# Kernel tuning notes

Measured on AMD Instinct MI355X. Metric: run time of the kernel, lower is better.

The kernel has to match this reference:

```python
import jax, jax.numpy as jnp
import numpy as np

B, T, C, H, HS = 2, 2048, 1024, 16, 64


def setup_inputs() -> dict:
    key = jax.random.key(0)
    ks = jax.random.split(key, 7)
    x = jax.random.normal(ks[0], (B, T, C), dtype=jnp.float32)
    # causal mask, broadcast over batch (True = attend)
    attention_mask = jnp.broadcast_to(jnp.tril(jnp.ones((T, T), dtype=bool)), (B, T, T))
    s = 1.0 / np.sqrt(C)
    wq = jax.random.normal(ks[1], (H, C, HS), dtype=jnp.float32) * s   # per-head query Linear (no bias)
    wk = jax.random.normal(ks[2], (H, C, HS), dtype=jnp.float32) * s
    wv = jax.random.normal(ks[3], (H, C, HS), dtype=jnp.float32) * s
    wproj = jax.random.normal(ks[4], (H * HS, C), dtype=jnp.float32) * (1.0 / np.sqrt(H * HS))
    bproj = jnp.zeros((C,), dtype=jnp.float32)
    return {"x": x, "attention_mask": attention_mask,
            "wq": wq, "wk": wk, "wv": wv, "wproj": wproj, "bproj": bproj}


def reference(x, attention_mask, wq, wk, wv, wproj, bproj):
    # per-head projections: [B,H,T,HS]
    q = jnp.einsum('btc,hcd->bhtd', x, wq)
    k = jnp.einsum('btc,hcd->bhtd', x, wk)
    v = jnp.einsum('btc,hcd->bhtd', x, wv)
    scale = 1.0 / jnp.sqrt(jnp.asarray(HS, dtype=x.dtype))
    wei = jnp.einsum('bhtd,bhsd->bhts', q, k) * scale          # [B,H,T,T]
    wei = jnp.where(attention_mask[:, None, :, :], wei, -jnp.inf)
    wei = jax.nn.softmax(wei, axis=-1)
    out = jnp.einsum('bhts,bhsd->bhtd', wei, v)                 # [B,H,T,HS]
    out = out.transpose(0, 2, 1, 3).reshape(B, T, H * HS)       # concat heads
    return out @ wproj + bproj                                  # [B,T,C]
```

## Files before the change

### kernel.cpp

```cpp
#include <hip/hip_runtime.h>
#include <math.h>

typedef float f32x4 __attribute__((ext_vector_type(4)));
typedef __bf16 bf16x8 __attribute__((ext_vector_type(8)));
typedef unsigned short u16x8 __attribute__((ext_vector_type(8)));
typedef unsigned short u16x4 __attribute__((ext_vector_type(4)));

#define DEV static __device__ __forceinline__

DEV unsigned short f2bf(float f) {
    unsigned int u = __builtin_bit_cast(unsigned int, f);
    u += 0x7fffu + ((u >> 16) & 1u);
    return (unsigned short)(u >> 16);
}

#define GLD16(gp, lp) __builtin_amdgcn_global_load_lds( \
    (__attribute__((address_space(1))) void*)(gp),      \
    (__attribute__((address_space(3))) void*)(lp), 16, 0, 0)

#define WAITBAR(N) asm volatile("s_waitcnt vmcnt(" #N ")\n\ts_barrier" ::: "memory")
#define BARRIER()  asm volatile("s_barrier" ::: "memory")

__global__ __launch_bounds__(256) void k_prep(const float* __restrict__ x,
                                              const float* __restrict__ wq,
                                              const float* __restrict__ wk,
                                              const float* __restrict__ wv,
                                              const float* __restrict__ wproj,
                                              unsigned short* __restrict__ xb,
                                              unsigned short* __restrict__ WqkvT,
                                              unsigned short* __restrict__ WprojT) {
    const int bid = blockIdx.x, tid = threadIdx.x;
    if (bid < 2048) {
        int i = bid * 256 + tid;
        const float4* p = (const float4*)(x + (size_t)i * 8);
        float4 a = p[0], b = p[1];
        u16x8 o;
        o[0] = f2bf(a.x); o[1] = f2bf(a.y); o[2] = f2bf(a.z); o[3] = f2bf(a.w);
        o[4] = f2bf(b.x); o[5] = f2bf(b.y); o[6] = f2bf(b.z); o[7] = f2bf(b.w);
        *(u16x8*)(xb + (size_t)i * 8) = o;
        return;
    }
    __shared__ unsigned short t[64][68];
    if (bid < 2816) {
        int zb = bid - 2048;
        int z = zb >> 4, wsel = z >> 4, zz = z & 15;
        const float* src = (wsel == 0 ? wq : wsel == 1 ? wk : wv) + (size_t)zz * 65536;
        int r0 = (zb & 15) * 64;
#pragma unroll
        for (int it = 0; it < 4; ++it) {
            int r = (tid >> 4) + it * 16;
            int c4 = (tid & 15) * 4;
            float4 v = *(const float4*)&src[(size_t)(r0 + r) * 64 + c4];
            t[c4 + 0][r] = f2bf(v.x);
            t[c4 + 1][r] = f2bf(v.y);
            t[c4 + 2][r] = f2bf(v.z);
            t[c4 + 3][r] = f2bf(v.w);
        }
        __syncthreads();
#pragma unroll
        for (int it = 0; it < 4; ++it) {
            int c = (tid >> 4) + it * 16;
            int r4 = (tid & 15) * 4;
            u16x4 o;
            o[0] = t[c][r4 + 0]; o[1] = t[c][r4 + 1];
            o[2] = t[c][r4 + 2]; o[3] = t[c][r4 + 3];
            int row = wsel * 1024 + zz * 64 + c;
            *(u16x4*)&WqkvT[(size_t)row * 1024 + r0 + r4] = o;
        }
    } else {
        int zb = bid - 2816;
        int r0 = (zb & 15) * 64, c0 = (zb >> 4) * 64;
#pragma unroll
        for (int it = 0; it < 4; ++it) {
            int r = (tid >> 4) + it * 16;
            int c4 = (tid & 15) * 4;
            float4 v = *(const float4*)&wproj[(size_t)(r0 + r) * 1024 + c0 + c4];
            t[c4 + 0][r] = f2bf(v.x);
            t[c4 + 1][r] = f2bf(v.y);
            t[c4 + 2][r] = f2bf(v.z);
            t[c4 + 3][r] = f2bf(v.w);
        }
        __syncthreads();
#pragma unroll
        for (int it = 0; it < 4; ++it) {
            int c = (tid >> 4) + it * 16;
            int r4 = (tid & 15) * 4;
            u16x4 o;
            o[0] = t[c][r4 + 0]; o[1] = t[c][r4 + 1];
            o[2] = t[c][r4 + 2]; o[3] = t[c][r4 + 3];
            *(u16x4*)&WprojT[(size_t)(c0 + c) * 1024 + r0 + r4] = o;
        }
    }
}

template <int STAGE, int M_REP, int NB, int SUPM, int SUPN>
__global__ __launch_bounds__(256) void k_gemm(const unsigned short* __restrict__ A,
                                              const unsigned short* __restrict__ Bt,
                                              int Kd,
                                              float* __restrict__ outF,
                                              const float* __restrict__ bias,
                                              unsigned short* __restrict__ Qb,
                                              unsigned short* __restrict__ Kb,
                                              unsigned short* __restrict__ Vt) {
    constexpr int BM = M_REP * 32;
    __shared__ unsigned short As[2][BM * 64] __attribute__((aligned(16)));
    __shared__ unsigned short Bs[2][128 * 64] __attribute__((aligned(16)));
    const int tid = threadIdx.x, l = tid & 63, w = tid >> 6;
    constexpr int BN_CH = NB / SUPN;
    const int orig = blockIdx.x;
    const int xcd = orig & 7, sdx = orig >> 3;
    const int bm = (xcd / BN_CH) * SUPM + (sdx % SUPM);
    const int bn = (xcd % BN_CH) * SUPN + (sdx / SUPM);
    const int wr = w >> 1, wc = w & 1;
    const int g = l >> 4, q = l & 15;
    f32x4 acc[M_REP][4] = {};
    const unsigned short* gA = A + (size_t)(bm * BM + w * 8 + (l >> 3)) * Kd + (l & 7) * 8;
    const unsigned short* gB = Bt + (size_t)(bn * 128 + w * 8 + (l >> 3)) * Kd + (l & 7) * 8;

#define GSTAGE(buf, k0) do {                                                  \
        _Pragma("unroll")                                                     \
        for (int it = 0; it < M_REP; ++it)                                    \
            GLD16(gA + (size_t)(it * 32) * Kd + (k0), &As[buf][(it * 32 + w * 8) * 64]); \
        _Pragma("unroll")                                                     \
        for (int it = 0; it < 4; ++it)                                        \
            GLD16(gB + (size_t)(it * 32) * Kd + (k0), &Bs[buf][(it * 32 + w * 8) * 64]); \
    } while (0)

    const int nt = Kd >> 6;
    GSTAGE(0, 0);
    int cur = 0;
    for (int t = 0; t < nt; ++t) {
        if (t + 1 < nt) {
            GSTAGE(cur ^ 1, (t + 1) << 6);
            if constexpr (M_REP == 4) WAITBAR(8); else WAITBAR(6);
        } else {
            WAITBAR(0);
        }
#pragma unroll
        for (int ks = 0; ks < 2; ++ks) {
            bf16x8 af[M_REP], bfr[4];
#pragma unroll
            for (int mi = 0; mi < M_REP; ++mi)
                af[mi] = *(const bf16x8*)&As[cur][(wr * (M_REP * 16) + mi * 16 + q) * 64 + ks * 32 + g * 8];
#pragma unroll
            for (int ni = 0; ni < 4; ++ni)
                bfr[ni] = *(const bf16x8*)&Bs[cur][(wc * 64 + ni * 16 + q) * 64 + ks * 32 + g * 8];
#pragma unroll
            for (int mi = 0; mi < M_REP; ++mi)
#pragma unroll
                for (int ni = 0; ni < 4; ++ni)
                    acc[mi][ni] = __builtin_amdgcn_mfma_f32_16x16x32_bf16(
                        af[mi], bfr[ni], acc[mi][ni], 0, 0, 0);
        }
        BARRIER();
        cur ^= 1;
    }
#undef GSTAGE
#pragma unroll
    for (int mi = 0; mi < M_REP; ++mi)
#pragma unroll
        for (int ni = 0; ni < 4; ++ni)
#pragma unroll
            for (int r = 0; r < 4; ++r) {
                float c = acc[mi][ni][r];
                int m = bm * BM + wr * (M_REP * 16) + mi * 16 + g * 4 + r;
                int n = bn * 128 + wc * 64 + ni * 16 + q;
                if (STAGE == 1) {
                    int b = m >> 11, t = m & 2047;
                    int proj = n >> 10, rr = n & 1023, h = rr >> 6, d = rr & 63;
                    int bh = b * 16 + h;
                    if (proj == 0)
                        Qb[((size_t)bh * 2048 + t) * 64 + d] = f2bf(c * 0.18033688011112042f);
                    else if (proj == 1)
                        Kb[((size_t)bh * 2048 + t) * 64 + d] = f2bf(c);
                    else
                        Vt[((size_t)bh * 64 + d) * 2048 + t] = f2bf(c);
                } else {
                    outF[(size_t)m * 1024 + n] = c + bias[n];
                }
            }
}

__global__ __launch_bounds__(256) void k_attn(const unsigned short* __restrict__ Qb,
                                              const unsigned short* __restrict__ Kb,
                                              const unsigned short* __restrict__ Vt,
                                              unsigned short* __restrict__ att) {
    __shared__ unsigned short Ks[2][2][4096] __attribute__((aligned(16)));
    __shared__ unsigned short Vs[2][2][4096] __attribute__((aligned(16)));
    __shared__ unsigned short P[4][16][72];
    const int tid = threadIdx.x, l = tid & 63, w = tid >> 6;
    const int pj = blockIdx.x, bh = blockIdx.y;
    const int b = bh >> 4, h = bh & 15;
    const int ql = l & 15, g = l >> 4;
    const unsigned short* Qp = Qb + (size_t)bh * 2048 * 64;
    const unsigned short* Kp = Kb + (size_t)bh * 2048 * 64;
    const unsigned short* Vp = Vt + (size_t)bh * 64 * 2048;

    const int sr0 = w * 16 + (l >> 3);
    const int sch = (l & 7) ^ (l >> 3);
    const unsigned short* gK0 = Kp + (size_t)sr0 * 64 + sch * 8;
    const unsigned short* gK1 = gK0 + 8 * 64;
    const unsigned short* gV0 = Vp + (size_t)sr0 * 2048 + sch * 8;
    const unsigned short* gV1 = gV0 + 8 * 2048;

#define ATT_STAGE(buf, kvb) do {                                                  \
        GLD16(gK0 + (size_t)(kvb) * 64, &Ks[buf][0][(w * 16) * 64]);              \
        GLD16(gK1 + (size_t)(kvb) * 64, &Ks[buf][0][(w * 16 + 8) * 64]);          \
        GLD16(gK0 + (size_t)((kvb) + 64) * 64, &Ks[buf][1][(w * 16) * 64]);       \
        GLD16(gK1 + (size_t)((kvb) + 64) * 64, &Ks[buf][1][(w * 16 + 8) * 64]);   \
        GLD16(gV0 + (kvb), &Vs[buf][0][(w * 16) * 64]);                           \
        GLD16(gV1 + (kvb), &Vs[buf][0][(w * 16 + 8) * 64]);                       \
        GLD16(gV0 + (kvb) + 64, &Vs[buf][1][(w * 16) * 64]);                      \
        GLD16(gV1 + (kvb) + 64, &Vs[buf][1][(w * 16 + 8) * 64]);                  \
    } while (0)

    for (int ph = 0; ph < 2; ++ph) {
        const int qt = ph ? (31 - pj) : pj;
        const int qg = qt * 64 + w * 16 + ql;
        const int minqg = qt * 64 + w * 16;
        const int nkv2 = (qt + 2) >> 1;

        bf16x8 qf0 = *(const bf16x8*)(Qp + (size_t)qg * 64 + g * 8);
        bf16x8 qf1 = *(const bf16x8*)(Qp + (size_t)qg * 64 + 32 + g * 8);
        f32x4 ot[4] = {};
        float mrun = -1e30f, lsum = 0.f;

        ATT_STAGE(0, 0);
        int cur = 0;

        for (int kb = 0; kb < nkv2; ++kb) {
            if (kb + 1 < nkv2) {
                ATT_STAGE(cur ^ 1, (kb + 1) * 128);
                WAITBAR(8);
            } else {
                WAITBAR(0);
            }
#pragma unroll
            for (int sub = 0; sub < 2; ++sub) {
                const int kvb = kb * 128 + sub * 64;
                const unsigned short* Kt = &Ks[cur][sub][0];
                const unsigned short* Vtl = &Vs[cur][sub][0];
                f32x4 st[4] = {};
                bf16x8 kf0[4], kf1[4];
#pragma unroll
                for (int f = 0; f < 4; ++f) {
                    int rk = f * 16 + ql, sw = rk & 7;
                    kf0[f] = *(const bf16x8*)&Kt[rk * 64 + ((g ^ sw) * 8)];
                    kf1[f] = *(const bf16x8*)&Kt[rk * 64 + (((g + 4) ^ sw) * 8)];
                }
                __builtin_amdgcn_s_setprio(1);
#pragma unroll
                for (int f = 0; f < 4; ++f) {
                    st[f] = __builtin_amdgcn_mfma_f32_16x16x32_bf16(kf0[f], qf0, st[f], 0, 0, 0);
                    st[f] = __builtin_amdgcn_mfma_f32_16x16x32_bf16(kf1[f], qf1, st[f], 0, 0, 0);
                }
                __builtin_amdgcn_s_setprio(0);
                if (kvb + 63 > minqg) {
#pragma unroll
                    for (int f = 0; f < 4; ++f)
#pragma unroll
                        for (int r = 0; r < 4; ++r)
                            if (kvb + f * 16 + g * 4 + r > qg) st[f][r] = -1e30f;
                }
                float pmax = -1e30f;
#pragma unroll
                for (int f = 0; f < 4; ++f)
#pragma unroll
                    for (int r = 0; r < 4; ++r) pmax = fmaxf(pmax, st[f][r]);
                if (!__all(pmax <= mrun + 8.f)) {
                    float pm = fmaxf(pmax, __shfl_xor(pmax, 16));
                    pm = fmaxf(pm, __shfl_xor(pm, 32));
                    float mnew = fmaxf(mrun, pm);
                    float corr = __builtin_amdgcn_exp2f(mrun - mnew);
                    lsum *= corr;
#pragma unroll
                    for (int f = 0; f < 4; ++f) ot[f] *= corr;
                    mrun = mnew;
                }
                float psum = 0.f;
#pragma unroll
                for (int f = 0; f < 4; ++f) {
                    u16x4 pk;
#pragma unroll
                    for (int r = 0; r < 4; ++r) {
                        float p = __builtin_amdgcn_exp2f(st[f][r] - mrun);
                        psum += p;
                        pk[r] = f2bf(p);
                    }
                    *(u16x4*)&P[w][ql][f * 16 + g * 4] = pk;
                }
                lsum += psum;
                asm volatile("s_waitcnt lgkmcnt(0)" ::: "memory");
#pragma unroll
                for (int dc = 0; dc < 2; ++dc) {
                    bf16x8 pf = *(const bf16x8*)&P[w][ql][dc * 32 + g * 8];
                    __builtin_amdgcn_s_setprio(1);
#pragma unroll
                    for (int f = 0; f < 4; ++f) {
                        int rv = f * 16 + ql, sw = rv & 7;
                        bf16x8 vf = *(const bf16x8*)&Vtl[rv * 64 + (((dc * 4 + g) ^ sw) * 8)];
                        ot[f] = __builtin_amdgcn_mfma_f32_16x16x32_bf16(vf, pf, ot[f], 0, 0, 0);
                    }
                    __builtin_amdgcn_s_setprio(0);
                }
            }
            BARRIER();
            cur ^= 1;
        }
        lsum += __shfl_xor(lsum, 16);
        lsum += __shfl_xor(lsum, 32);
        float inv = 1.f / lsum;
        unsigned short* ap = att + ((size_t)(b * 2048 + qg)) * 1024 + h * 64;
#pragma unroll
        for (int f = 0; f < 4; ++f) {
            u16x4 o;
#pragma unroll
            for (int r = 0; r < 4; ++r) o[r] = f2bf(ot[f][r] * inv);
            *(u16x4*)&ap[f * 16 + g * 4] = o;
        }
    }
#undef ATT_STAGE
}

extern "C" void kernel_launch(void* const* d_in, const int* in_sizes, int n_in,
                              void* d_out, int out_size, void* d_ws, size_t ws_size,
                              hipStream_t stream) {
    const float* x = (const float*)d_in[0];
    const float* wq = (const float*)d_in[2];
    const float* wk = (const float*)d_in[3];
    const float* wv = (const float*)d_in[4];
    const float* wproj = (const float*)d_in[5];
    const float* bproj = (const float*)d_in[6];
    float* out = (float*)d_out;

    char* ws = (char*)d_ws;
    unsigned short* xb     = (unsigned short*)(ws);
    unsigned short* WqkvT  = (unsigned short*)(ws + (8u << 20));
    unsigned short* WprojT = (unsigned short*)(ws + (14u << 20));
    unsigned short* Qb     = (unsigned short*)(ws + (16u << 20));
    unsigned short* Kb     = (unsigned short*)(ws + (24u << 20));
    unsigned short* Vt     = (unsigned short*)(ws + (32u << 20));
    unsigned short* att    = xb;

    k_prep<<<3072, 256, 0, stream>>>(x, wq, wk, wv, wproj, xb, WqkvT, WprojT);
    k_gemm<1, 4, 24, 8, 12><<<768, 256, 0, stream>>>(xb, WqkvT, 1024, nullptr, nullptr, Qb, Kb, Vt);
    k_attn<<<dim3(16, 32), 256, 0, stream>>>(Qb, Kb, Vt, att);
    k_gemm<3, 2, 8, 16, 4><<<512, 256, 0, stream>>>(att, WprojT, 1024, out, bproj, nullptr, nullptr, nullptr);
}
```

Before: 133.8 us.

## Process two 16-row query blocks per wave to reuse K/V fragments

Each wave now handles 32 query rows (two 16-row groups) instead of 16, so every K and V fragment read from LDS feeds two sets of MFMAs. The attention grid shrinks from 16 to 8 query-tile pairs per head-batch, and 64-key sub-blocks lying entirely above the causal diagonal are skipped. This lowers LDS reads and global K/V staging per query. In exchange it raises register pressure, halves the block count, which may reduce occupancy and parallelism, and serializes both query groups through the single per-wave P buffer.

Result: slower. 147.3 us (+10.1%).

```diff
diff --git a/kernel.cpp b/kernel.cpp
--- a/kernel.cpp
+++ b/kernel.cpp
@@ -215,15 +215,19 @@
     } while (0)
 
     for (int ph = 0; ph < 2; ++ph) {
-        const int qt = ph ? (31 - pj) : pj;
-        const int qg = qt * 64 + w * 16 + ql;
-        const int minqg = qt * 64 + w * 16;
-        const int nkv2 = (qt + 2) >> 1;
-
-        bf16x8 qf0 = *(const bf16x8*)(Qp + (size_t)qg * 64 + g * 8);
-        bf16x8 qf1 = *(const bf16x8*)(Qp + (size_t)qg * 64 + 32 + g * 8);
-        f32x4 ot[4] = {};
-        float mrun = -1e30f, lsum = 0.f;
+        const int qt = ph ? (15 - pj) : pj;
+        const int base = qt * 128 + w * 32;
+        const int maxqg = base + 31;
+        const int nkv2 = qt + 1;
+
+        bf16x8 qf[2][2];
+#pragma unroll
+        for (int qi = 0; qi < 2; ++qi) {
+            qf[qi][0] = *(const bf16x8*)(Qp + (size_t)(base + qi * 16 + ql) * 64 + g * 8);
+            qf[qi][1] = *(const bf16x8*)(Qp + (size_t)(base + qi * 16 + ql) * 64 + 32 + g * 8);
+        }
+        f32x4 ot[2][4] = {};
+        float mrun[2] = {-1e30f, -1e30f}, lsum[2] = {0.f, 0.f};
 
         ATT_STAGE(0, 0);
         int cur = 0;
@@ -238,85 +242,99 @@
 #pragma unroll
             for (int sub = 0; sub < 2; ++sub) {
                 const int kvb = kb * 128 + sub * 64;
-                const unsigned short* Kt = &Ks[cur][sub][0];
-                const unsigned short* Vtl = &Vs[cur][sub][0];
-                f32x4 st[4] = {};
-                bf16x8 kf0[4], kf1[4];
-#pragma unroll
-                for (int f = 0; f < 4; ++f) {
-                    int rk = f * 16 + ql, sw = rk & 7;
-                    kf0[f] = *(const bf16x8*)&Kt[rk * 64 + ((g ^ sw) * 8)];
-                    kf1[f] = *(const bf16x8*)&Kt[rk * 64 + (((g + 4) ^ sw) * 8)];
-                }
-                __builtin_amdgcn_s_setprio(1);
-#pragma unroll
-                for (int f = 0; f < 4; ++f) {
-                    st[f] = __builtin_amdgcn_mfma_f32_16x16x32_bf16(kf0[f], qf0, st[f], 0, 0, 0);
-                    st[f] = __builtin_amdgcn_mfma_f32_16x16x32_bf16(kf1[f], qf1, st[f], 0, 0, 0);
-                }
-                __builtin_amdgcn_s_setprio(0);
-                if (kvb + 63 > minqg) {
+                if (kvb <= maxqg) {
+                    const unsigned short* Kt = &Ks[cur][sub][0];
+                    const unsigned short* Vtl = &Vs[cur][sub][0];
+                    bf16x8 kf0[4], kf1[4], vfr[2][4];
+#pragma unroll
+                    for (int f = 0; f < 4; ++f) {
+                        int rk = f * 16 + ql, sw = rk & 7;
+                        kf0[f] = *(const bf16x8*)&Kt[rk * 64 + ((g ^ sw) * 8)];
+                        kf1[f] = *(const bf16x8*)&Kt[rk * 64 + (((g + 4) ^ sw) * 8)];
+#pragma unroll
+                        for (int dc = 0; dc < 2; ++dc)
+                            vfr[dc][f] = *(const bf16x8*)&Vtl[rk * 64 + (((dc * 4 + g) ^ sw) * 8)];
+                    }
+                    f32x4 st[2][4] = {};
+                    __builtin_amdgcn_s_setprio(1);
 #pragma unroll
                     for (int f = 0; f < 4; ++f)
 #pragma unroll
-                        for (int r = 0; r < 4; ++r)
-                            if (kvb + f * 16 + g * 4 + r > qg) st[f][r] = -1e30f;
-                }
-                float pmax = -1e30f;
-#pragma unroll
-                for (int f = 0; f < 4; ++f)
-#pragma unroll
-                    for (int r = 0; r < 4; ++r) pmax = fmaxf(pmax, st[f][r]);
-                if (!__all(pmax <= mrun + 8.f)) {
-                    float pm = fmaxf(pmax, __shfl_xor(pmax, 16));
-                    pm = fmaxf(pm, __shfl_xor(pm, 32));
-                    float mnew = fmaxf(mrun, pm);
-                    float corr = __builtin_amdgcn_exp2f(mrun - mnew);
-                    lsum *= corr;
-#pragma unroll
-                    for (int f = 0; f < 4; ++f) ot[f] *= corr;
-                    mrun = mnew;
-                }
-                float psum = 0.f;
-#pragma unroll
-                for (int f = 0; f < 4; ++f) {
-                    u16x4 pk;
-#pragma unroll
-                    for (int r = 0; r < 4; ++r) {
-                        float p = __builtin_amdgcn_exp2f(st[f][r] - mrun);
-                        psum += p;
-                        pk[r] = f2bf(p);
+                        for (int qi = 0; qi < 2; ++qi) {
+                            st[qi][f] = __builtin_amdgcn_mfma_f32_16x16x32_bf16(kf0[f], qf[qi][0], st[qi][f], 0, 0, 0);
+                            st[qi][f] = __builtin_amdgcn_mfma_f32_16x16x32_bf16(kf1[f], qf[qi][1], st[qi][f], 0, 0, 0);
+                        }
+                    __builtin_amdgcn_s_setprio(0);
+                    const bool needmask = (kvb + 63 > base);
+#pragma unroll
+                    for (int qi = 0; qi < 2; ++qi) {
+                        const int qg = base + qi * 16 + ql;
+                        if (needmask) {
+#pragma unroll
+                            for (int f = 0; f < 4; ++f)
+#pragma unroll
+                                for (int r = 0; r < 4; ++r)
+                                    if (kvb + f * 16 + g * 4 + r > qg) st[qi][f][r] = -1e30f;
+                        }
+                        float pmax = -1e30f;
+#pragma unroll
+                        for (int f = 0; f < 4; ++f)
+#pragma unroll
+                            for (int r = 0; r < 4; ++r) pmax = fmaxf(pmax, st[qi][f][r]);
+                        if (!__all(pmax <= mrun[qi] + 8.f)) {
+                            float pm = fmaxf(pmax, __shfl_xor(pmax, 16));
+                            pm = fmaxf(pm, __shfl_xor(pm, 32));
+                            float mnew = fmaxf(mrun[qi], pm);
+                            float corr = __builtin_amdgcn_exp2f(mrun[qi] - mnew);
+                            lsum[qi] *= corr;
+#pragma unroll
+                            for (int f = 0; f < 4; ++f) ot[qi][f] *= corr;
+                            mrun[qi] = mnew;
+                        }
+                        float psum = 0.f;
+#pragma unroll
+                        for (int f = 0; f < 4; ++f) {
+                            u16x4 pk;
+#pragma unroll
+                            for (int r = 0; r < 4; ++r) {
+                                float p = __builtin_amdgcn_exp2f(st[qi][f][r] - mrun[qi]);
+                                psum += p;
+                                pk[r] = f2bf(p);
+                            }
+                            *(u16x4*)&P[w][ql][f * 16 + g * 4] = pk;
+                        }
+                        lsum[qi] += psum;
+                        asm volatile("s_waitcnt lgkmcnt(0)" ::: "memory");
+#pragma unroll
+                        for (int dc = 0; dc < 2; ++dc) {
+                            bf16x8 pf = *(const bf16x8*)&P[w][ql][dc * 32 + g * 8];
+                            __builtin_amdgcn_s_setprio(1);
+#pragma unroll
+                            for (int f = 0; f < 4; ++f)
+                                ot[qi][f] = __builtin_amdgcn_mfma_f32_16x16x32_bf16(vfr[dc][f], pf, ot[qi][f], 0, 0, 0);
+                            __builtin_amdgcn_s_setprio(0);
+                        }
                     }
-                    *(u16x4*)&P[w][ql][f * 16 + g * 4] = pk;
-                }
-                lsum += psum;
-                asm volatile("s_waitcnt lgkmcnt(0)" ::: "memory");
-#pragma unroll
-                for (int dc = 0; dc < 2; ++dc) {
-                    bf16x8 pf = *(const bf16x8*)&P[w][ql][dc * 32 + g * 8];
-                    __builtin_amdgcn_s_setprio(1);
-#pragma unroll
-                    for (int f = 0; f < 4; ++f) {
-                        int rv = f * 16 + ql, sw = rv & 7;
-                        bf16x8 vf = *(const bf16x8*)&Vtl[rv * 64 + (((dc * 4 + g) ^ sw) * 8)];
-                        ot[f] = __builtin_amdgcn_mfma_f32_16x16x32_bf16(vf, pf, ot[f], 0, 0, 0);
-                    }
-                    __builtin_amdgcn_s_setprio(0);
                 }
             }
             BARRIER();
             cur ^= 1;
         }
-        lsum += __shfl_xor(lsum, 16);
-        lsum += __shfl_xor(lsum, 32);
-        float inv = 1.f / lsum;
-        unsigned short* ap = att + ((size_t)(b * 2048 + qg)) * 1024 + h * 64;
-#pragma unroll
-        for (int f = 0; f < 4; ++f) {
-            u16x4 o;
-#pragma unroll
-            for (int r = 0; r < 4; ++r) o[r] = f2bf(ot[f][r] * inv);
-            *(u16x4*)&ap[f * 16 + g * 4] = o;
+#pragma unroll
+        for (int qi = 0; qi < 2; ++qi) {
+            float ls = lsum[qi];
+            ls += __shfl_xor(ls, 16);
+            ls += __shfl_xor(ls, 32);
+            float inv = 1.f / ls;
+            const int qg = base + qi * 16 + ql;
+            unsigned short* ap = att + ((size_t)(b * 2048 + qg)) * 1024 + h * 64;
+#pragma unroll
+            for (int f = 0; f < 4; ++f) {
+                u16x4 o;
+#pragma unroll
+                for (int r = 0; r < 4; ++r) o[r] = f2bf(ot[qi][f][r] * inv);
+                *(u16x4*)&ap[f * 16 + g * 4] = o;
+            }
         }
     }
 #undef ATT_STAGE
@@ -344,6 +362,6 @@
 
     k_prep<<<3072, 256, 0, stream>>>(x, wq, wk, wv, wproj, xb, WqkvT, WprojT);
     k_gemm<1, 4, 24, 8, 12><<<768, 256, 0, stream>>>(xb, WqkvT, 1024, nullptr, nullptr, Qb, Kb, Vt);
-    k_attn<<<dim3(16, 32), 256, 0, stream>>>(Qb, Kb, Vt, att);
+    k_attn<<<dim3(8, 32), 256, 0, stream>>>(Qb, Kb, Vt, att);
     k_gemm<3, 2, 8, 16, 4><<<512, 256, 0, stream>>>(att, WprojT, 1024, out, bproj, nullptr, nullptr, nullptr);
 }
```
